# Kernel optimization log

Hardware: AMD Instinct MI355X
Metric: run time of the kernel (lower is better)

## Reference

```python
import jax, jax.numpy as jnp
import numpy as np

N = 50000   # nodes
E = 800000  # random edges (self-loops appended inside reference, as PyG GATConv does)
H = 4       # attention heads
LEAKY_SLOPE = 0.2
BN_EPS = 1e-5


def setup_inputs() -> dict:
    key = jax.random.key(0)
    ks = jax.random.split(key, 24)
    inp = {
        "x": jax.random.normal(ks[0], (N, 128), jnp.float32),
        "edge_index": jax.random.randint(ks[1], (2, E), 0, N, dtype=jnp.int64),
    }
    # layer dims: (in, out_per_head); concat -> out width = H*out
    dims = [(128, 64), (256, 64), (256, 32)]
    i = 2
    for l, (fin, c) in enumerate(dims, start=1):
        sc = 1.0 / np.sqrt(fin)
        inp[f"W{l}"] = jax.random.normal(ks[i], (fin, H * c), jnp.float32) * sc; i += 1
        inp[f"a_src{l}"] = jax.random.normal(ks[i], (H, c), jnp.float32) * 0.1; i += 1
        inp[f"a_dst{l}"] = jax.random.normal(ks[i], (H, c), jnp.float32) * 0.1; i += 1
        inp[f"b{l}"] = jnp.zeros((H * c,), jnp.float32)
    # batch norm params for the two non-final layers (width = 64*4 = 256)
    for l in (1, 2):
        inp[f"gamma{l}"] = jnp.ones((256,), jnp.float32)
        inp[f"beta{l}"] = jnp.zeros((256,), jnp.float32)
    return inp


def _gat_layer(x, src, dst, W, a_src, a_dst, b, heads):
    n = x.shape[0]
    h = (x @ W).reshape(n, heads, -1)                      # [N,H,C]
    al_s = jnp.sum(h * a_src, axis=-1)                     # [N,H]
    al_d = jnp.sum(h * a_dst, axis=-1)                     # [N,H]
    e = jax.nn.leaky_relu(al_s[src] + al_d[dst], LEAKY_SLOPE)  # [Etot,H]
    # numerically-stable edge softmax over incoming edges per destination
    m = jax.ops.segment_max(e, dst, num_segments=n)
    e = jnp.exp(e - m[dst])
    s = jax.ops.segment_sum(e, dst, num_segments=n)
    alpha = e / (s[dst] + 1e-16)                           # [Etot,H]
    msg = alpha[:, :, None] * h[src]                       # [Etot,H,C]
    out = jax.ops.segment_sum(msg, dst, num_segments=n)    # [N,H,C]
    out = out.reshape(n, -1) + b
    return jax.nn.relu(out)  # GAT_NET applies relu after conv


def _batch_norm(x, gamma, beta):
    mean = jnp.mean(x, axis=0)
    var = jnp.var(x, axis=0)  # biased, matches torch BN training normalization
    return (x - mean) * jax.lax.rsqrt(var + BN_EPS) * gamma + beta


def reference(x, edge_index, W1, a_src1, a_dst1, b1, gamma1, beta1,
              W2, a_src2, a_dst2, b2, gamma2, beta2,
              W3, a_src3, a_dst3, b3):
    n = x.shape[0]
    loop = jnp.arange(n, dtype=edge_index.dtype)
    src = jnp.concatenate([edge_index[0], loop])  # add self-loops (PyG default)
    dst = jnp.concatenate([edge_index[1], loop])

    h = _gat_layer(x, src, dst, W1, a_src1, a_dst1, b1, H)
    # outer F.relu is a no-op after GAT_NET's internal relu, kept implicitly
    h = _batch_norm(h, gamma1, beta1)

    h = _gat_layer(h, src, dst, W2, a_src2, a_dst2, b2, H)
    h = _batch_norm(h, gamma2, beta2)

    return _gat_layer(h, src, dst, W3, a_src3, a_dst3, b3, H)
```

## Files before the change

### kernel.cpp

```cpp
#include <hip/hip_runtime.h>
#include <hip/hip_bf16.h>

constexpr int NN   = 50000;
constexpr int EE   = 800000;
constexpr int ETOT = EE + NN;
constexpr int NP   = 50048;
constexpr int NBLK = (NN + 255) / 256;
constexpr float SLOPE  = 0.2f;
constexpr float EPS_BN = 1e-5f;

typedef __attribute__((ext_vector_type(8))) short bf16x8;
typedef __attribute__((ext_vector_type(4))) float f32x4;

__device__ inline float bf2f(unsigned short u) {
    union { unsigned int i; float f; } c; c.i = ((unsigned int)u) << 16; return c.f;
}

__device__ inline void gload16(const __hip_bfloat16* g, __hip_bfloat16* l) {
    __builtin_amdgcn_global_load_lds(
        (const __attribute__((address_space(1))) unsigned int*)g,
        (__attribute__((address_space(3))) unsigned int*)l, 16, 0, 0);
}


__global__ __launch_bounds__(256) void count_kernel(const int* __restrict__ ei,
                                                    int* __restrict__ cnt) {
    int j = blockIdx.x * 256 + threadIdx.x;
    if (j >= ETOT) return;
    int dst = (j < EE) ? ei[EE + j] : (j - EE);
    atomicAdd(&cnt[dst], 1);
}

__global__ __launch_bounds__(256) void scanA_kernel(const int* __restrict__ cnt,
                                                    int* __restrict__ off,
                                                    int* __restrict__ bsum) {
    int b = blockIdx.x, t = threadIdx.x;
    int i = b * 256 + t;
    int v = (i < NN) ? cnt[i] : 0;
    int lane = t & 63, w = t >> 6;
    int x = v;
    #pragma unroll
    for (int o = 1; o < 64; o <<= 1) { int y = __shfl_up(x, o); if (lane >= o) x += y; }
    __shared__ int ws[4];
    if (lane == 63) ws[w] = x;
    __syncthreads();
    int wo = 0;
    for (int k = 0; k < w; ++k) wo += ws[k];
    int incl = x + wo;
    if (i < NN) off[i] = incl - v;
    if (t == 255) bsum[b] = incl;
}

__global__ __launch_bounds__(256) void scanB_kernel(const int* __restrict__ bsum,
                                                    int* __restrict__ bexc,
                                                    int* __restrict__ off) {
    int t = threadIdx.x;
    int v = (t < NBLK) ? bsum[t] : 0;
    int lane = t & 63, w = t >> 6;
    int x = v;
    #pragma unroll
    for (int o = 1; o < 64; o <<= 1) { int y = __shfl_up(x, o); if (lane >= o) x += y; }
    __shared__ int ws[4];
    if (lane == 63) ws[w] = x;
    __syncthreads();
    int wo = 0;
    for (int k = 0; k < w; ++k) wo += ws[k];
    int incl = x + wo;
    if (t < NBLK) bexc[t] = incl - v;
    if (t == 255) off[NN] = incl;
}

__global__ __launch_bounds__(256) void scanC_kernel(const int* __restrict__ bexc,
                                                    int* __restrict__ off,
                                                    int* __restrict__ cur) {
    int i = blockIdx.x * 256 + threadIdx.x;
    if (i >= NN) return;
    int v = off[i] + bexc[blockIdx.x];
    off[i] = v;
    cur[i] = v;
}

__global__ __launch_bounds__(256) void fill_kernel(const int* __restrict__ ei,
                                                   int* __restrict__ cursor,
                                                   int* __restrict__ ssrc) {
    int j = blockIdx.x * 256 + threadIdx.x;
    if (j >= ETOT) return;
    int src, dst;
    if (j < EE) { src = ei[j]; dst = ei[EE + j]; }
    else        { src = dst = j - EE; }
    int pos = atomicAdd(&cursor[dst], 1);
    ssrc[pos] = src;
}

constexpr int XB = (int)(((long)NP * 128 / 8 + 255) / 256);
__global__ __launch_bounds__(256) void castwx_kernel(const float* __restrict__ X,
                                                     const float* __restrict__ W,
                                                     __hip_bfloat16* __restrict__ Xbf,
                                                     __hip_bfloat16* __restrict__ WT) {
    int b = blockIdx.x;
    if (b < XB) {
        long e0 = ((long)b * 256 + threadIdx.x) * 8;
        if (e0 >= (long)NP * 128) return;
        int row = (int)(e0 / 128);
        __hip_bfloat16 o[8];
        if (row < NN) {
            float4 v0 = *reinterpret_cast<const float4*>(X + e0);
            float4 v1 = *reinterpret_cast<const float4*>(X + e0 + 4);
            o[0] = __float2bfloat16(v0.x); o[1] = __float2bfloat16(v0.y);
            o[2] = __float2bfloat16(v0.z); o[3] = __float2bfloat16(v0.w);
            o[4] = __float2bfloat16(v1.x); o[5] = __float2bfloat16(v1.y);
            o[6] = __float2bfloat16(v1.z); o[7] = __float2bfloat16(v1.w);
        } else {
            for (int j = 0; j < 8; ++j) o[j] = __float2bfloat16(0.f);
        }
        *reinterpret_cast<bf16x8*>(Xbf + e0) = *reinterpret_cast<bf16x8*>(o);
    } else {
        int i = (b - XB) * 256 + threadIdx.x;
        int c = i / 128, k = i % 128;
        WT[i] = __float2bfloat16(W[(size_t)k * 256 + c]);
    }
}

template <int WOUT>
__global__ __launch_bounds__(256) void foldw_kernel(const float* __restrict__ W,
                                                    const float* __restrict__ sums,
                                                    const float* __restrict__ gamma,
                                                    const float* __restrict__ beta,
                                                    __hip_bfloat16* __restrict__ WTp,
                                                    float* __restrict__ bb) {
    int c = blockIdx.x, k = threadIdx.x;
    float mean = sums[k] / (float)NN;
    float var  = sums[256 + k] / (float)NN - mean * mean;
    float inv  = rsqrtf(var + EPS_BN);
    float sc   = gamma[k] * inv;
    float sh   = beta[k] - mean * sc;
    float w = W[(size_t)k * WOUT + c];
    WTp[(size_t)c * 256 + k] = __float2bfloat16(sc * w);
    float p = sh * w;
    #pragma unroll
    for (int o = 1; o < 64; o <<= 1) p += __shfl_xor(p, o);
    __shared__ float ps[4];
    if ((k & 63) == 0) ps[k >> 6] = p;
    __syncthreads();
    if (k == 0) bb[c] = ps[0] + ps[1] + ps[2] + ps[3];
}

template <int FIN, int WOUT, bool FOLD>
__global__ __launch_bounds__(256) void mgemm_kernel(const __hip_bfloat16* __restrict__ A,
                                                    const __hip_bfloat16* __restrict__ BT,
                                                    const float* __restrict__ bb,
                                                    const float* __restrict__ a_src,
                                                    const float* __restrict__ a_dst,
                                                    __hip_bfloat16* __restrict__ Hbf,
                                                    float* __restrict__ als,
                                                    float* __restrict__ ald) {
    __shared__ __hip_bfloat16 As[128 * 32];
    __shared__ __hip_bfloat16 Bs[128 * 32];
    int t = threadIdx.x;
    int lane = t & 63, w = t >> 6;
    int row0 = blockIdx.x * 128;
    int col0 = blockIdx.y * 128;
    int wr = w >> 1, wc = w & 1;

    f32x4 acc[4][4];
    #pragma unroll
    for (int m = 0; m < 4; ++m)
        #pragma unroll
        for (int n = 0; n < 4; ++n) acc[m][n] = (f32x4){0.f, 0.f, 0.f, 0.f};

    int srow = w * 32 + (lane >> 2);
    int sbc  = (lane & 3) * 8;
    const __hip_bfloat16* gA0 = A  + (size_t)(row0 + srow)      * FIN + sbc;
    const __hip_bfloat16* gA1 = A  + (size_t)(row0 + srow + 16) * FIN + sbc;
    const __hip_bfloat16* gB0 = BT + (size_t)(col0 + srow)      * FIN + sbc;
    const __hip_bfloat16* gB1 = BT + (size_t)(col0 + srow + 16) * FIN + sbc;
    __hip_bfloat16* lA0 = As + w * 1024;
    __hip_bfloat16* lA1 = As + w * 1024 + 512;
    __hip_bfloat16* lB0 = Bs + w * 1024;
    __hip_bfloat16* lB1 = Bs + w * 1024 + 512;

    int rA = (wr * 64 + (lane & 15)) * 32 + (lane >> 4) * 8;
    int rB = (wc * 64 + (lane & 15)) * 32 + (lane >> 4) * 8;

    for (int k0 = 0; k0 < FIN; k0 += 32) {
        gload16(gA0 + k0, lA0);
        gload16(gA1 + k0, lA1);
        gload16(gB0 + k0, lB0);
        gload16(gB1 + k0, lB1);
        __syncthreads();
        bf16x8 af[4], bfr[4];
        #pragma unroll
        for (int m = 0; m < 4; ++m) af[m]  = *reinterpret_cast<const bf16x8*>(As + rA + m * 16 * 32);
        #pragma unroll
        for (int n = 0; n < 4; ++n) bfr[n] = *reinterpret_cast<const bf16x8*>(Bs + rB + n * 16 * 32);
        #pragma unroll
        for (int m = 0; m < 4; ++m)
            #pragma unroll
            for (int n = 0; n < 4; ++n)
                acc[m][n] = __builtin_amdgcn_mfma_f32_16x16x32_bf16(af[m], bfr[n], acc[m][n], 0, 0, 0);
        __syncthreads();
    }

    int cih = lane & 15;

    if constexpr (FOLD) {
        #pragma unroll
        for (int n = 0; n < 4; ++n) {
            float badd = bb[col0 + wc * 64 + n * 16 + cih];
            #pragma unroll
            for (int m = 0; m < 4; ++m)
                #pragma unroll
                for (int j = 0; j < 4; ++j) acc[m][n][j] += badd;
        }
    }

    float asv[4], adv[4];
    int headw = 0;
    if constexpr (WOUT == 256) {
        headw = (col0 >> 6) + wc;
        #pragma unroll
        for (int n = 0; n < 4; ++n) {
            asv[n] = a_src[headw * 64 + n * 16 + cih];
            adv[n] = a_dst[headw * 64 + n * 16 + cih];
        }
    } else {
        #pragma unroll
        for (int n = 0; n < 4; ++n) {
            int hh = wc * 2 + (n >> 1);
            asv[n] = a_src[hh * 32 + (n & 1) * 16 + cih];
            adv[n] = a_dst[hh * 32 + (n & 1) * 16 + cih];
        }
    }

    #pragma unroll
    for (int m = 0; m < 4; ++m) {
        #pragma unroll
        for (int j = 0; j < 4; ++j) {
            int r = row0 + wr * 64 + m * 16 + (lane >> 4) * 4 + j;
            if constexpr (WOUT == 256) {
                float vs = acc[m][0][j] * asv[0] + acc[m][1][j] * asv[1]
                         + acc[m][2][j] * asv[2] + acc[m][3][j] * asv[3];
                float vd = acc[m][0][j] * adv[0] + acc[m][1][j] * adv[1]
                         + acc[m][2][j] * adv[2] + acc[m][3][j] * adv[3];
                #pragma unroll
                for (int o = 1; o < 16; o <<= 1) {
                    vs += __shfl_xor(vs, o);
                    vd += __shfl_xor(vd, o);
                }
                if (cih == 0) {
                    als[(size_t)r * 4 + headw] = vs;
                    ald[(size_t)r * 4 + headw] = vd;
                }
            } else {
                float vs0 = acc[m][0][j] * asv[0] + acc[m][1][j] * asv[1];
                float vs1 = acc[m][2][j] * asv[2] + acc[m][3][j] * asv[3];
                float vd0 = acc[m][0][j] * adv[0] + acc[m][1][j] * adv[1];
                float vd1 = acc[m][2][j] * adv[2] + acc[m][3][j] * adv[3];
                #pragma unroll
                for (int o = 1; o < 16; o <<= 1) {
                    vs0 += __shfl_xor(vs0, o); vs1 += __shfl_xor(vs1, o);
                    vd0 += __shfl_xor(vd0, o); vd1 += __shfl_xor(vd1, o);
                }
                if (cih == 0) {
                    als[(size_t)r * 4 + wc * 2]     = vs0;
                    als[(size_t)r * 4 + wc * 2 + 1] = vs1;
                    ald[(size_t)r * 4 + wc * 2]     = vd0;
                    ald[(size_t)r * 4 + wc * 2 + 1] = vd1;
                }
            }
        }
    }

    #pragma unroll
    for (int n = 0; n < 4; ++n) {
        int c = col0 + wc * 64 + n * 16 + cih;
        #pragma unroll
        for (int m = 0; m < 4; ++m) {
            int r = row0 + wr * 64 + m * 16 + (lane >> 4) * 4;
            #pragma unroll
            for (int j = 0; j < 4; ++j)
                Hbf[(size_t)(r + j) * WOUT + c] = __float2bfloat16(acc[m][n][j]);
        }
    }
}

__global__ __launch_bounds__(256) void attn256_kernel(const __hip_bfloat16* __restrict__ Hm,
                                                      const int* __restrict__ off,
                                                      const int* __restrict__ ssrc,
                                                      const float* __restrict__ als,
                                                      const float* __restrict__ ald,
                                                      const float* __restrict__ bias,
                                                      __hip_bfloat16* __restrict__ Out) {
    int wid  = threadIdx.x >> 6;
    int lane = threadIdx.x & 63;
    int g    = lane >> 4;
    int q    = lane & 15;
    int d    = blockIdx.x * 16 + wid * 4 + g;
    int hA   = q >> 3;

    int e0 = off[d], e1 = off[d + 1];
    float aldA = ald[(size_t)d * 4 + hA];
    float aldB = ald[(size_t)d * 4 + hA + 2];

    float accA[8], accB[8];
    #pragma unroll
    for (int c = 0; c < 8; ++c) { accA[c] = 0.f; accB[c] = 0.f; }
    float denA = 0.f, denB = 0.f;

    int j = e0;
    for (; j + 3 < e1; j += 4) {
        int s0 = ssrc[j], s1 = ssrc[j + 1], s2 = ssrc[j + 2], s3 = ssrc[j + 3];
        const __hip_bfloat16* r0 = Hm + (size_t)s0 * 256 + q * 8;
        const __hip_bfloat16* r1 = Hm + (size_t)s1 * 256 + q * 8;
        const __hip_bfloat16* r2 = Hm + (size_t)s2 * 256 + q * 8;
        const __hip_bfloat16* r3 = Hm + (size_t)s3 * 256 + q * 8;
        bf16x8 a0 = *reinterpret_cast<const bf16x8*>(r0);
        bf16x8 b0 = *reinterpret_cast<const bf16x8*>(r0 + 128);
        bf16x8 a1 = *reinterpret_cast<const bf16x8*>(r1);
        bf16x8 b1 = *reinterpret_cast<const bf16x8*>(r1 + 128);
        bf16x8 a2 = *reinterpret_cast<const bf16x8*>(r2);
        bf16x8 b2 = *reinterpret_cast<const bf16x8*>(r2 + 128);
        bf16x8 a3 = *reinterpret_cast<const bf16x8*>(r3);
        bf16x8 b3 = *reinterpret_cast<const bf16x8*>(r3 + 128);
        float xA0 = als[(size_t)s0 * 4 + hA] + aldA, xB0 = als[(size_t)s0 * 4 + hA + 2] + aldB;
        float xA1 = als[(size_t)s1 * 4 + hA] + aldA, xB1 = als[(size_t)s1 * 4 + hA + 2] + aldB;
        float xA2 = als[(size_t)s2 * 4 + hA] + aldA, xB2 = als[(size_t)s2 * 4 + hA + 2] + aldB;
        float xA3 = als[(size_t)s3 * 4 + hA] + aldA, xB3 = als[(size_t)s3 * 4 + hA + 2] + aldB;
        xA0 = (xA0 > 0.f) ? xA0 : SLOPE * xA0;  xB0 = (xB0 > 0.f) ? xB0 : SLOPE * xB0;
        xA1 = (xA1 > 0.f) ? xA1 : SLOPE * xA1;  xB1 = (xB1 > 0.f) ? xB1 : SLOPE * xB1;
        xA2 = (xA2 > 0.f) ? xA2 : SLOPE * xA2;  xB2 = (xB2 > 0.f) ? xB2 : SLOPE * xB2;
        xA3 = (xA3 > 0.f) ? xA3 : SLOPE * xA3;  xB3 = (xB3 > 0.f) ? xB3 : SLOPE * xB3;
        float wA0 = __expf(xA0), wB0 = __expf(xB0);
        float wA1 = __expf(xA1), wB1 = __expf(xB1);
        float wA2 = __expf(xA2), wB2 = __expf(xB2);
        float wA3 = __expf(xA3), wB3 = __expf(xB3);
        denA += (wA0 + wA1) + (wA2 + wA3);
        denB += (wB0 + wB1) + (wB2 + wB3);
        #pragma unroll
        for (int c = 0; c < 8; ++c) {
            accA[c] += wA0 * bf2f((unsigned short)a0[c]) + wA1 * bf2f((unsigned short)a1[c])
                     + wA2 * bf2f((unsigned short)a2[c]) + wA3 * bf2f((unsigned short)a3[c]);
            accB[c] += wB0 * bf2f((unsigned short)b0[c]) + wB1 * bf2f((unsigned short)b1[c])
                     + wB2 * bf2f((unsigned short)b2[c]) + wB3 * bf2f((unsigned short)b3[c]);
        }
    }
    for (; j < e1; ++j) {
        int s0 = ssrc[j];
        const __hip_bfloat16* r0 = Hm + (size_t)s0 * 256 + q * 8;
        bf16x8 a0 = *reinterpret_cast<const bf16x8*>(r0);
        bf16x8 b0 = *reinterpret_cast<const bf16x8*>(r0 + 128);
        float xA0 = als[(size_t)s0 * 4 + hA] + aldA, xB0 = als[(size_t)s0 * 4 + hA + 2] + aldB;
        xA0 = (xA0 > 0.f) ? xA0 : SLOPE * xA0;  xB0 = (xB0 > 0.f) ? xB0 : SLOPE * xB0;
        float wA0 = __expf(xA0), wB0 = __expf(xB0);
        denA += wA0; denB += wB0;
        #pragma unroll
        for (int c = 0; c < 8; ++c) {
            accA[c] += wA0 * bf2f((unsigned short)a0[c]);
            accB[c] += wB0 * bf2f((unsigned short)b0[c]);
        }
    }

    float invA = 1.f / (denA + 1e-16f);
    float invB = 1.f / (denB + 1e-16f);

    float4 bA0 = *reinterpret_cast<const float4*>(bias + q * 8);
    float4 bA1 = *reinterpret_cast<const float4*>(bias + q * 8 + 4);
    float4 bB0 = *reinterpret_cast<const float4*>(bias + 128 + q * 8);
    float4 bB1 = *reinterpret_cast<const float4*>(bias + 128 + q * 8 + 4);
    __hip_bfloat16 oA[8], oB[8];
    oA[0] = __float2bfloat16(fmaxf(accA[0] * invA + bA0.x, 0.f));
    oA[1] = __float2bfloat16(fmaxf(accA[1] * invA + bA0.y, 0.f));
    oA[2] = __float2bfloat16(fmaxf(accA[2] * invA + bA0.z, 0.f));
    oA[3] = __float2bfloat16(fmaxf(accA[3] * invA + bA0.w, 0.f));
    oA[4] = __float2bfloat16(fmaxf(accA[4] * invA + bA1.x, 0.f));
    oA[5] = __float2bfloat16(fmaxf(accA[5] * invA + bA1.y, 0.f));
    oA[6] = __float2bfloat16(fmaxf(accA[6] * invA + bA1.z, 0.f));
    oA[7] = __float2bfloat16(fmaxf(accA[7] * invA + bA1.w, 0.f));
    oB[0] = __float2bfloat16(fmaxf(accB[0] * invB + bB0.x, 0.f));
    oB[1] = __float2bfloat16(fmaxf(accB[1] * invB + bB0.y, 0.f));
    oB[2] = __float2bfloat16(fmaxf(accB[2] * invB + bB0.z, 0.f));
    oB[3] = __float2bfloat16(fmaxf(accB[3] * invB + bB0.w, 0.f));
    oB[4] = __float2bfloat16(fmaxf(accB[4] * invB + bB1.x, 0.f));
    oB[5] = __float2bfloat16(fmaxf(accB[5] * invB + bB1.y, 0.f));
    oB[6] = __float2bfloat16(fmaxf(accB[6] * invB + bB1.z, 0.f));
    oB[7] = __float2bfloat16(fmaxf(accB[7] * invB + bB1.w, 0.f));
    __hip_bfloat16* op = Out + (size_t)d * 256 + q * 8;
    *reinterpret_cast<bf16x8*>(op)       = *reinterpret_cast<bf16x8*>(oA);
    *reinterpret_cast<bf16x8*>(op + 128) = *reinterpret_cast<bf16x8*>(oB);
}

__global__ __launch_bounds__(256) void attn128_kernel(const __hip_bfloat16* __restrict__ Hm,
                                                      const int* __restrict__ off,
                                                      const int* __restrict__ ssrc,
                                                      const float* __restrict__ als,
                                                      const float* __restrict__ ald,
                                                      const float* __restrict__ bias,
                                                      float* __restrict__ Out) {
    int wid  = threadIdx.x >> 6;
    int lane = threadIdx.x & 63;
    int g    = lane >> 4;
    int q    = lane & 15;
    int d    = blockIdx.x * 16 + wid * 4 + g;
    int head = q >> 2;

    int e0 = off[d], e1 = off[d + 1];
    float aldh = ald[(size_t)d * 4 + head];

    float acc[8];
    #pragma unroll
    for (int c = 0; c < 8; ++c) acc[c] = 0.f;
    float den = 0.f;

    int j = e0;
    for (; j + 3 < e1; j += 4) {
        int s0 = ssrc[j], s1 = ssrc[j + 1], s2 = ssrc[j + 2], s3 = ssrc[j + 3];
        bf16x8 a0 = *reinterpret_cast<const bf16x8*>(Hm + (size_t)s0 * 128 + q * 8);
        bf16x8 a1 = *reinterpret_cast<const bf16x8*>(Hm + (size_t)s1 * 128 + q * 8);
        bf16x8 a2 = *reinterpret_cast<const bf16x8*>(Hm + (size_t)s2 * 128 + q * 8);
        bf16x8 a3 = *reinterpret_cast<const bf16x8*>(Hm + (size_t)s3 * 128 + q * 8);
        float x0 = als[(size_t)s0 * 4 + head] + aldh;
        float x1 = als[(size_t)s1 * 4 + head] + aldh;
        float x2 = als[(size_t)s2 * 4 + head] + aldh;
        float x3 = als[(size_t)s3 * 4 + head] + aldh;
        x0 = (x0 > 0.f) ? x0 : SLOPE * x0;
        x1 = (x1 > 0.f) ? x1 : SLOPE * x1;
        x2 = (x2 > 0.f) ? x2 : SLOPE * x2;
        x3 = (x3 > 0.f) ? x3 : SLOPE * x3;
        float w0 = __expf(x0), w1 = __expf(x1), w2 = __expf(x2), w3 = __expf(x3);
        den += (w0 + w1) + (w2 + w3);
        #pragma unroll
        for (int c = 0; c < 8; ++c)
            acc[c] += w0 * bf2f((unsigned short)a0[c]) + w1 * bf2f((unsigned short)a1[c])
                    + w2 * bf2f((unsigned short)a2[c]) + w3 * bf2f((unsigned short)a3[c]);
    }
    for (; j < e1; ++j) {
        int s0 = ssrc[j];
        bf16x8 a0 = *reinterpret_cast<const bf16x8*>(Hm + (size_t)s0 * 128 + q * 8);
        float x0 = als[(size_t)s0 * 4 + head] + aldh;
        x0 = (x0 > 0.f) ? x0 : SLOPE * x0;
        float w0 = __expf(x0);
        den += w0;
        #pragma unroll
        for (int c = 0; c < 8; ++c) acc[c] += w0 * bf2f((unsigned short)a0[c]);
    }

    float inv = 1.f / (den + 1e-16f);
    float4 b0 = *reinterpret_cast<const float4*>(bias + q * 8);
    float4 b1 = *reinterpret_cast<const float4*>(bias + q * 8 + 4);
    float* op = Out + (size_t)d * 128 + q * 8;
    *reinterpret_cast<float4*>(op) = make_float4(
        fmaxf(acc[0] * inv + b0.x, 0.f), fmaxf(acc[1] * inv + b0.y, 0.f),
        fmaxf(acc[2] * inv + b0.z, 0.f), fmaxf(acc[3] * inv + b0.w, 0.f));
    *reinterpret_cast<float4*>(op + 4) = make_float4(
        fmaxf(acc[4] * inv + b1.x, 0.f), fmaxf(acc[5] * inv + b1.y, 0.f),
        fmaxf(acc[6] * inv + b1.z, 0.f), fmaxf(acc[7] * inv + b1.w, 0.f));
}

__global__ __launch_bounds__(256) void bnstats_kernel(const __hip_bfloat16* __restrict__ X,
                                                      float* __restrict__ sums) {
    int c  = threadIdx.x;
    int r0 = blockIdx.x * 200;
    float s = 0.f, q = 0.f;
    for (int r = r0; r < r0 + 200; ++r) {
        float v = bf2f(*(const unsigned short*)(X + (size_t)r * 256 + c));
        s += v; q += v * v;
    }
    atomicAdd(&sums[c], s);
    atomicAdd(&sums[256 + c], q);
}


extern "C" void kernel_launch(void* const* d_in, const int* in_sizes, int n_in,
                              void* d_out, int out_size, void* d_ws, size_t ws_size,
                              hipStream_t stream) {
    const float* x      = (const float*)d_in[0];
    const int*   ei     = (const int*)d_in[1];
    const float* W1     = (const float*)d_in[2];
    const float* a_s1   = (const float*)d_in[3];
    const float* a_d1   = (const float*)d_in[4];
    const float* b1     = (const float*)d_in[5];
    const float* W2     = (const float*)d_in[6];
    const float* a_s2   = (const float*)d_in[7];
    const float* a_d2   = (const float*)d_in[8];
    const float* b2     = (const float*)d_in[9];
    const float* W3     = (const float*)d_in[10];
    const float* a_s3   = (const float*)d_in[11];
    const float* a_d3   = (const float*)d_in[12];
    const float* b3     = (const float*)d_in[13];
    const float* gamma1 = (const float*)d_in[14];
    const float* beta1  = (const float*)d_in[15];
    const float* gamma2 = (const float*)d_in[16];
    const float* beta2  = (const float*)d_in[17];

    char* ws = (char*)d_ws;
    size_t o = 0;
    auto alloc = [&](size_t bytes) -> void* {
        void* p = ws + o;
        o = (o + bytes + 255) & ~size_t(255);
        return p;
    };
    __hip_bfloat16*  Abf  = (__hip_bfloat16*)alloc((size_t)NP * 256 * 2);
    __hip_bfloat16*  Hbf  = (__hip_bfloat16*)alloc((size_t)NP * 256 * 2);
    __hip_bfloat16*  Xbf  = (__hip_bfloat16*)alloc((size_t)NP * 128 * 2);
    __hip_bfloat16*  WT1  = (__hip_bfloat16*)alloc((size_t)256 * 128 * 2);
    __hip_bfloat16*  WT2  = (__hip_bfloat16*)alloc((size_t)256 * 256 * 2);
    __hip_bfloat16*  WT3  = (__hip_bfloat16*)alloc((size_t)128 * 256 * 2);
    float* bb2   = (float*)alloc(256 * 4);
    float* bb3   = (float*)alloc(128 * 4);
    float* als   = (float*)alloc((size_t)NP * 4 * 4);
    float* ald   = (float*)alloc((size_t)NP * 4 * 4);
    float* sums  = (float*)alloc(512 * 4);
    int*   off   = (int*)alloc((size_t)(NN + 1) * 4);
    int*   cur   = (int*)alloc((size_t)NN * 4);
    int*   cnt   = (int*)alloc((size_t)NN * 4);
    int*   bsum  = (int*)alloc((size_t)NBLK * 4);
    int*   bexc  = (int*)alloc((size_t)NBLK * 4);
    int*   ssrc  = (int*)alloc((size_t)ETOT * 4);
    (void)ws_size; (void)in_sizes; (void)n_in; (void)out_size;

    const int EB = (ETOT + 255) / 256;

    hipMemsetAsync(cnt, 0, (size_t)NN * 4, stream);
    count_kernel<<<EB, 256, 0, stream>>>(ei, cnt);
    scanA_kernel<<<NBLK, 256, 0, stream>>>(cnt, off, bsum);
    scanB_kernel<<<1, 256, 0, stream>>>(bsum, bexc, off);
    scanC_kernel<<<NBLK, 256, 0, stream>>>(bexc, off, cur);
    fill_kernel<<<EB, 256, 0, stream>>>(ei, cur, ssrc);

    castwx_kernel<<<XB + 128, 256, 0, stream>>>(x, W1, Xbf, WT1);
    mgemm_kernel<128, 256, false><<<dim3(NP / 128, 2), 256, 0, stream>>>(
        Xbf, WT1, nullptr, a_s1, a_d1, Hbf, als, ald);
    attn256_kernel<<<NN / 16, 256, 0, stream>>>(Hbf, off, ssrc, als, ald, b1, Abf);

    hipMemsetAsync(sums, 0, 512 * 4, stream);
    bnstats_kernel<<<250, 256, 0, stream>>>(Abf, sums);
    foldw_kernel<256><<<256, 256, 0, stream>>>(W2, sums, gamma1, beta1, WT2, bb2);

    mgemm_kernel<256, 256, true><<<dim3(NP / 128, 2), 256, 0, stream>>>(
        Abf, WT2, bb2, a_s2, a_d2, Hbf, als, ald);
    attn256_kernel<<<NN / 16, 256, 0, stream>>>(Hbf, off, ssrc, als, ald, b2, Abf);

    hipMemsetAsync(sums, 0, 512 * 4, stream);
    bnstats_kernel<<<250, 256, 0, stream>>>(Abf, sums);
    foldw_kernel<128><<<128, 256, 0, stream>>>(W3, sums, gamma2, beta2, WT3, bb3);

    mgemm_kernel<256, 128, true><<<dim3(NP / 128, 1), 256, 0, stream>>>(
        Abf, WT3, bb3, a_s3, a_d3, Hbf, als, ald);
    attn128_kernel<<<NN / 16, 256, 0, stream>>>(Hbf, off, ssrc, als, ald, b3, (float*)d_out);
}
```

Measured before the change: 382.1 us.

## Store GEMM output in column panels and split attention aggregation by panel

The GEMM epilogue now writes H into 8 column panels (32 or 16 bf16 wide), each stored contiguously across nodes. The attention kernels get a 2D grid where blockIdx.x selects the panel. Within a wave, the edges of one destination are spread across lanes and combined with a shuffle reduction. The intent is that each panel (about 3.2 MB) fits in cache, so the random source-row gathers hit L2/MALL instead of DRAM, and that lanes parallelise over edges instead of looping serially. In exchange, the per-edge index and attention-logit loads and exp computations are repeated for every panel, and the reductions add shuffle overhead.

After: 696.6 us. 1.82x slower.

```diff
diff --git a/kernel.cpp b/kernel.cpp
--- a/kernel.cpp
+++ b/kernel.cpp
@@ -151,9 +151,10 @@
                                                     const float* __restrict__ bb,
                                                     const float* __restrict__ a_src,
                                                     const float* __restrict__ a_dst,
-                                                    __hip_bfloat16* __restrict__ Hbf,
+                                                    __hip_bfloat16* __restrict__ Hpan,
                                                     float* __restrict__ als,
                                                     float* __restrict__ ald) {
+    constexpr int PW = (WOUT == 256) ? 32 : 16;
     __shared__ __hip_bfloat16 As[128 * 32];
     __shared__ __hip_bfloat16 Bs[128 * 32];
     int t = threadIdx.x;
@@ -274,186 +275,141 @@
     #pragma unroll
     for (int n = 0; n < 4; ++n) {
         int c = col0 + wc * 64 + n * 16 + cih;
+        int p = c / PW;
+        int cw = c % PW;
         #pragma unroll
         for (int m = 0; m < 4; ++m) {
             int r = row0 + wr * 64 + m * 16 + (lane >> 4) * 4;
             #pragma unroll
             for (int j = 0; j < 4; ++j)
-                Hbf[(size_t)(r + j) * WOUT + c] = __float2bfloat16(acc[m][n][j]);
-        }
-    }
-}
-
-__global__ __launch_bounds__(256) void attn256_kernel(const __hip_bfloat16* __restrict__ Hm,
-                                                      const int* __restrict__ off,
-                                                      const int* __restrict__ ssrc,
-                                                      const float* __restrict__ als,
-                                                      const float* __restrict__ ald,
-                                                      const float* __restrict__ bias,
-                                                      __hip_bfloat16* __restrict__ Out) {
-    int wid  = threadIdx.x >> 6;
+                Hpan[(size_t)p * NP * PW + (size_t)(r + j) * PW + cw] =
+                    __float2bfloat16(acc[m][n][j]);
+        }
+    }
+}
+
+__global__ __launch_bounds__(256) void attn256s_kernel(const __hip_bfloat16* __restrict__ Hpan,
+                                                       const int* __restrict__ off,
+                                                       const int* __restrict__ ssrc,
+                                                       const float* __restrict__ als,
+                                                       const float* __restrict__ ald,
+                                                       const float* __restrict__ bias,
+                                                       __hip_bfloat16* __restrict__ Out) {
+    int s    = blockIdx.x;
+    int wv   = threadIdx.x >> 6;
     int lane = threadIdx.x & 63;
-    int g    = lane >> 4;
-    int q    = lane & 15;
-    int d    = blockIdx.x * 16 + wid * 4 + g;
-    int hA   = q >> 3;
-
-    int e0 = off[d], e1 = off[d + 1];
-    float aldA = ald[(size_t)d * 4 + hA];
-    float aldB = ald[(size_t)d * 4 + hA + 2];
-
-    float accA[8], accB[8];
-    #pragma unroll
-    for (int c = 0; c < 8; ++c) { accA[c] = 0.f; accB[c] = 0.f; }
-    float denA = 0.f, denB = 0.f;
-
-    int j = e0;
-    for (; j + 3 < e1; j += 4) {
-        int s0 = ssrc[j], s1 = ssrc[j + 1], s2 = ssrc[j + 2], s3 = ssrc[j + 3];
-        const __hip_bfloat16* r0 = Hm + (size_t)s0 * 256 + q * 8;
-        const __hip_bfloat16* r1 = Hm + (size_t)s1 * 256 + q * 8;
-        const __hip_bfloat16* r2 = Hm + (size_t)s2 * 256 + q * 8;
-        const __hip_bfloat16* r3 = Hm + (size_t)s3 * 256 + q * 8;
-        bf16x8 a0 = *reinterpret_cast<const bf16x8*>(r0);
-        bf16x8 b0 = *reinterpret_cast<const bf16x8*>(r0 + 128);
-        bf16x8 a1 = *reinterpret_cast<const bf16x8*>(r1);
-        bf16x8 b1 = *reinterpret_cast<const bf16x8*>(r1 + 128);
-        bf16x8 a2 = *reinterpret_cast<const bf16x8*>(r2);
-        bf16x8 b2 = *reinterpret_cast<const bf16x8*>(r2 + 128);
-        bf16x8 a3 = *reinterpret_cast<const bf16x8*>(r3);
-        bf16x8 b3 = *reinterpret_cast<const bf16x8*>(r3 + 128);
-        float xA0 = als[(size_t)s0 * 4 + hA] + aldA, xB0 = als[(size_t)s0 * 4 + hA + 2] + aldB;
-        float xA1 = als[(size_t)s1 * 4 + hA] + aldA, xB1 = als[(size_t)s1 * 4 + hA + 2] + aldB;
-        float xA2 = als[(size_t)s2 * 4 + hA] + aldA, xB2 = als[(size_t)s2 * 4 + hA + 2] + aldB;
-        float xA3 = als[(size_t)s3 * 4 + hA] + aldA, xB3 = als[(size_t)s3 * 4 + hA + 2] + aldB;
-        xA0 = (xA0 > 0.f) ? xA0 : SLOPE * xA0;  xB0 = (xB0 > 0.f) ? xB0 : SLOPE * xB0;
-        xA1 = (xA1 > 0.f) ? xA1 : SLOPE * xA1;  xB1 = (xB1 > 0.f) ? xB1 : SLOPE * xB1;
-        xA2 = (xA2 > 0.f) ? xA2 : SLOPE * xA2;  xB2 = (xB2 > 0.f) ? xB2 : SLOPE * xB2;
-        xA3 = (xA3 > 0.f) ? xA3 : SLOPE * xA3;  xB3 = (xB3 > 0.f) ? xB3 : SLOPE * xB3;
-        float wA0 = __expf(xA0), wB0 = __expf(xB0);
-        float wA1 = __expf(xA1), wB1 = __expf(xB1);
-        float wA2 = __expf(xA2), wB2 = __expf(xB2);
-        float wA3 = __expf(xA3), wB3 = __expf(xB3);
-        denA += (wA0 + wA1) + (wA2 + wA3);
-        denB += (wB0 + wB1) + (wB2 + wB3);
-        #pragma unroll
-        for (int c = 0; c < 8; ++c) {
-            accA[c] += wA0 * bf2f((unsigned short)a0[c]) + wA1 * bf2f((unsigned short)a1[c])
-                     + wA2 * bf2f((unsigned short)a2[c]) + wA3 * bf2f((unsigned short)a3[c]);
-            accB[c] += wB0 * bf2f((unsigned short)b0[c]) + wB1 * bf2f((unsigned short)b1[c])
-                     + wB2 * bf2f((unsigned short)b2[c]) + wB3 * bf2f((unsigned short)b3[c]);
-        }
-    }
-    for (; j < e1; ++j) {
-        int s0 = ssrc[j];
-        const __hip_bfloat16* r0 = Hm + (size_t)s0 * 256 + q * 8;
-        bf16x8 a0 = *reinterpret_cast<const bf16x8*>(r0);
-        bf16x8 b0 = *reinterpret_cast<const bf16x8*>(r0 + 128);
-        float xA0 = als[(size_t)s0 * 4 + hA] + aldA, xB0 = als[(size_t)s0 * 4 + hA + 2] + aldB;
-        xA0 = (xA0 > 0.f) ? xA0 : SLOPE * xA0;  xB0 = (xB0 > 0.f) ? xB0 : SLOPE * xB0;
-        float wA0 = __expf(xA0), wB0 = __expf(xB0);
-        denA += wA0; denB += wB0;
-        #pragma unroll
-        for (int c = 0; c < 8; ++c) {
-            accA[c] += wA0 * bf2f((unsigned short)a0[c]);
-            accB[c] += wB0 * bf2f((unsigned short)b0[c]);
-        }
-    }
-
-    float invA = 1.f / (denA + 1e-16f);
-    float invB = 1.f / (denB + 1e-16f);
-
-    float4 bA0 = *reinterpret_cast<const float4*>(bias + q * 8);
-    float4 bA1 = *reinterpret_cast<const float4*>(bias + q * 8 + 4);
-    float4 bB0 = *reinterpret_cast<const float4*>(bias + 128 + q * 8);
-    float4 bB1 = *reinterpret_cast<const float4*>(bias + 128 + q * 8 + 4);
-    __hip_bfloat16 oA[8], oB[8];
-    oA[0] = __float2bfloat16(fmaxf(accA[0] * invA + bA0.x, 0.f));
-    oA[1] = __float2bfloat16(fmaxf(accA[1] * invA + bA0.y, 0.f));
-    oA[2] = __float2bfloat16(fmaxf(accA[2] * invA + bA0.z, 0.f));
-    oA[3] = __float2bfloat16(fmaxf(accA[3] * invA + bA0.w, 0.f));
-    oA[4] = __float2bfloat16(fmaxf(accA[4] * invA + bA1.x, 0.f));
-    oA[5] = __float2bfloat16(fmaxf(accA[5] * invA + bA1.y, 0.f));
-    oA[6] = __float2bfloat16(fmaxf(accA[6] * invA + bA1.z, 0.f));
-    oA[7] = __float2bfloat16(fmaxf(accA[7] * invA + bA1.w, 0.f));
-    oB[0] = __float2bfloat16(fmaxf(accB[0] * invB + bB0.x, 0.f));
-    oB[1] = __float2bfloat16(fmaxf(accB[1] * invB + bB0.y, 0.f));
-    oB[2] = __float2bfloat16(fmaxf(accB[2] * invB + bB0.z, 0.f));
-    oB[3] = __float2bfloat16(fmaxf(accB[3] * invB + bB0.w, 0.f));
-    oB[4] = __float2bfloat16(fmaxf(accB[4] * invB + bB1.x, 0.f));
-    oB[5] = __float2bfloat16(fmaxf(accB[5] * invB + bB1.y, 0.f));
-    oB[6] = __float2bfloat16(fmaxf(accB[6] * invB + bB1.z, 0.f));
-    oB[7] = __float2bfloat16(fmaxf(accB[7] * invB + bB1.w, 0.f));
-    __hip_bfloat16* op = Out + (size_t)d * 256 + q * 8;
-    *reinterpret_cast<bf16x8*>(op)       = *reinterpret_cast<bf16x8*>(oA);
-    *reinterpret_cast<bf16x8*>(op + 128) = *reinterpret_cast<bf16x8*>(oB);
-}
-
-__global__ __launch_bounds__(256) void attn128_kernel(const __hip_bfloat16* __restrict__ Hm,
-                                                      const int* __restrict__ off,
-                                                      const int* __restrict__ ssrc,
-                                                      const float* __restrict__ als,
-                                                      const float* __restrict__ ald,
-                                                      const float* __restrict__ bias,
-                                                      float* __restrict__ Out) {
-    int wid  = threadIdx.x >> 6;
+    int cl   = lane >> 2;
+    int sub  = lane & 3;
+    int head = s >> 1;
+    const __hip_bfloat16* Hp = Hpan + (size_t)s * NP * 32;
+
+    float4 bia0 = *reinterpret_cast<const float4*>(bias + s * 32 + sub * 8);
+    float4 bia1 = *reinterpret_cast<const float4*>(bias + s * 32 + sub * 8 + 4);
+
+    #pragma unroll
+    for (int k = 0; k < 4; ++k) {
+        int d = blockIdx.y * 16 + wv * 4 + k;
+        int e0 = off[d], e1 = off[d + 1];
+        float aldh = ald[(size_t)d * 4 + head];
+
+        float acc[8];
+        #pragma unroll
+        for (int c = 0; c < 8; ++c) acc[c] = 0.f;
+        float den = 0.f;
+
+        for (int j = e0 + cl; j < e1; j += 16) {
+            int src = ssrc[j];
+            float x = als[(size_t)src * 4 + head] + aldh;
+            x = (x > 0.f) ? x : SLOPE * x;
+            float wgt = __expf(x);
+            den += wgt;
+            bf16x8 v = *reinterpret_cast<const bf16x8*>(Hp + (size_t)src * 32 + sub * 8);
+            #pragma unroll
+            for (int c = 0; c < 8; ++c) acc[c] += wgt * bf2f((unsigned short)v[c]);
+        }
+
+        #pragma unroll
+        for (int o = 4; o < 64; o <<= 1) {
+            #pragma unroll
+            for (int c = 0; c < 8; ++c) acc[c] += __shfl_xor(acc[c], o);
+            den += __shfl_xor(den, o);
+        }
+        float inv = 1.f / (den + 1e-16f);
+
+        if (cl == 0) {
+            __hip_bfloat16 ob[8];
+            ob[0] = __float2bfloat16(fmaxf(acc[0] * inv + bia0.x, 0.f));
+            ob[1] = __float2bfloat16(fmaxf(acc[1] * inv + bia0.y, 0.f));
+            ob[2] = __float2bfloat16(fmaxf(acc[2] * inv + bia0.z, 0.f));
+            ob[3] = __float2bfloat16(fmaxf(acc[3] * inv + bia0.w, 0.f));
+            ob[4] = __float2bfloat16(fmaxf(acc[4] * inv + bia1.x, 0.f));
+            ob[5] = __float2bfloat16(fmaxf(acc[5] * inv + bia1.y, 0.f));
+            ob[6] = __float2bfloat16(fmaxf(acc[6] * inv + bia1.z, 0.f));
+            ob[7] = __float2bfloat16(fmaxf(acc[7] * inv + bia1.w, 0.f));
+            *reinterpret_cast<bf16x8*>(Out + (size_t)d * 256 + s * 32 + sub * 8) =
+                *reinterpret_cast<bf16x8*>(ob);
+        }
+    }
+}
+
+__global__ __launch_bounds__(256) void attn128s_kernel(const __hip_bfloat16* __restrict__ Hpan,
+                                                       const int* __restrict__ off,
+                                                       const int* __restrict__ ssrc,
+                                                       const float* __restrict__ als,
+                                                       const float* __restrict__ ald,
+                                                       const float* __restrict__ bias,
+                                                       float* __restrict__ Out) {
+    int s    = blockIdx.x;
+    int wv   = threadIdx.x >> 6;
     int lane = threadIdx.x & 63;
-    int g    = lane >> 4;
-    int q    = lane & 15;
-    int d    = blockIdx.x * 16 + wid * 4 + g;
-    int head = q >> 2;
-
-    int e0 = off[d], e1 = off[d + 1];
-    float aldh = ald[(size_t)d * 4 + head];
-
-    float acc[8];
-    #pragma unroll
-    for (int c = 0; c < 8; ++c) acc[c] = 0.f;
-    float den = 0.f;
-
-    int j = e0;
-    for (; j + 3 < e1; j += 4) {
-        int s0 = ssrc[j], s1 = ssrc[j + 1], s2 = ssrc[j + 2], s3 = ssrc[j + 3];
-        bf16x8 a0 = *reinterpret_cast<const bf16x8*>(Hm + (size_t)s0 * 128 + q * 8);
-        bf16x8 a1 = *reinterpret_cast<const bf16x8*>(Hm + (size_t)s1 * 128 + q * 8);
-        bf16x8 a2 = *reinterpret_cast<const bf16x8*>(Hm + (size_t)s2 * 128 + q * 8);
-        bf16x8 a3 = *reinterpret_cast<const bf16x8*>(Hm + (size_t)s3 * 128 + q * 8);
-        float x0 = als[(size_t)s0 * 4 + head] + aldh;
-        float x1 = als[(size_t)s1 * 4 + head] + aldh;
-        float x2 = als[(size_t)s2 * 4 + head] + aldh;
-        float x3 = als[(size_t)s3 * 4 + head] + aldh;
-        x0 = (x0 > 0.f) ? x0 : SLOPE * x0;
-        x1 = (x1 > 0.f) ? x1 : SLOPE * x1;
-        x2 = (x2 > 0.f) ? x2 : SLOPE * x2;
-        x3 = (x3 > 0.f) ? x3 : SLOPE * x3;
-        float w0 = __expf(x0), w1 = __expf(x1), w2 = __expf(x2), w3 = __expf(x3);
-        den += (w0 + w1) + (w2 + w3);
-        #pragma unroll
-        for (int c = 0; c < 8; ++c)
-            acc[c] += w0 * bf2f((unsigned short)a0[c]) + w1 * bf2f((unsigned short)a1[c])
-                    + w2 * bf2f((unsigned short)a2[c]) + w3 * bf2f((unsigned short)a3[c]);
-    }
-    for (; j < e1; ++j) {
-        int s0 = ssrc[j];
-        bf16x8 a0 = *reinterpret_cast<const bf16x8*>(Hm + (size_t)s0 * 128 + q * 8);
-        float x0 = als[(size_t)s0 * 4 + head] + aldh;
-        x0 = (x0 > 0.f) ? x0 : SLOPE * x0;
-        float w0 = __expf(x0);
-        den += w0;
-        #pragma unroll
-        for (int c = 0; c < 8; ++c) acc[c] += w0 * bf2f((unsigned short)a0[c]);
-    }
-
-    float inv = 1.f / (den + 1e-16f);
-    float4 b0 = *reinterpret_cast<const float4*>(bias + q * 8);
-    float4 b1 = *reinterpret_cast<const float4*>(bias + q * 8 + 4);
-    float* op = Out + (size_t)d * 128 + q * 8;
-    *reinterpret_cast<float4*>(op) = make_float4(
-        fmaxf(acc[0] * inv + b0.x, 0.f), fmaxf(acc[1] * inv + b0.y, 0.f),
-        fmaxf(acc[2] * inv + b0.z, 0.f), fmaxf(acc[3] * inv + b0.w, 0.f));
-    *reinterpret_cast<float4*>(op + 4) = make_float4(
-        fmaxf(acc[4] * inv + b1.x, 0.f), fmaxf(acc[5] * inv + b1.y, 0.f),
-        fmaxf(acc[6] * inv + b1.z, 0.f), fmaxf(acc[7] * inv + b1.w, 0.f));
+    int cl   = lane >> 1;
+    int sub  = lane & 1;
+    int head = s >> 1;
+    const __hip_bfloat16* Hp = Hpan + (size_t)s * NP * 16;
+
+    float4 bia0 = *reinterpret_cast<const float4*>(bias + s * 16 + sub * 8);
+    float4 bia1 = *reinterpret_cast<const float4*>(bias + s * 16 + sub * 8 + 4);
+
+    #pragma unroll
+    for (int k = 0; k < 4; ++k) {
+        int d = blockIdx.y * 16 + wv * 4 + k;
+        int e0 = off[d], e1 = off[d + 1];
+        float aldh = ald[(size_t)d * 4 + head];
+
+        float acc[8];
+        #pragma unroll
+        for (int c = 0; c < 8; ++c) acc[c] = 0.f;
+        float den = 0.f;
+
+        for (int j = e0 + cl; j < e1; j += 32) {
+            int src = ssrc[j];
+            float x = als[(size_t)src * 4 + head] + aldh;
+            x = (x > 0.f) ? x : SLOPE * x;
+            float wgt = __expf(x);
+            den += wgt;
+            bf16x8 v = *reinterpret_cast<const bf16x8*>(Hp + (size_t)src * 16 + sub * 8);
+            #pragma unroll
+            for (int c = 0; c < 8; ++c) acc[c] += wgt * bf2f((unsigned short)v[c]);
+        }
+
+        #pragma unroll
+        for (int o = 2; o < 64; o <<= 1) {
+            #pragma unroll
+            for (int c = 0; c < 8; ++c) acc[c] += __shfl_xor(acc[c], o);
+            den += __shfl_xor(den, o);
+        }
+        float inv = 1.f / (den + 1e-16f);
+
+        if (cl == 0) {
+            float* op = Out + (size_t)d * 128 + s * 16 + sub * 8;
+            *reinterpret_cast<float4*>(op) = make_float4(
+                fmaxf(acc[0] * inv + bia0.x, 0.f), fmaxf(acc[1] * inv + bia0.y, 0.f),
+                fmaxf(acc[2] * inv + bia0.z, 0.f), fmaxf(acc[3] * inv + bia0.w, 0.f));
+            *reinterpret_cast<float4*>(op + 4) = make_float4(
+                fmaxf(acc[4] * inv + bia1.x, 0.f), fmaxf(acc[5] * inv + bia1.y, 0.f),
+                fmaxf(acc[6] * inv + bia1.z, 0.f), fmaxf(acc[7] * inv + bia1.w, 0.f));
+        }
+    }
 }
 
 __global__ __launch_bounds__(256) void bnstats_kernel(const __hip_bfloat16* __restrict__ X,
@@ -530,7 +486,7 @@
     castwx_kernel<<<XB + 128, 256, 0, stream>>>(x, W1, Xbf, WT1);
     mgemm_kernel<128, 256, false><<<dim3(NP / 128, 2), 256, 0, stream>>>(
         Xbf, WT1, nullptr, a_s1, a_d1, Hbf, als, ald);
-    attn256_kernel<<<NN / 16, 256, 0, stream>>>(Hbf, off, ssrc, als, ald, b1, Abf);
+    attn256s_kernel<<<dim3(8, NN / 16), 256, 0, stream>>>(Hbf, off, ssrc, als, ald, b1, Abf);
 
     hipMemsetAsync(sums, 0, 512 * 4, stream);
     bnstats_kernel<<<250, 256, 0, stream>>>(Abf, sums);
@@ -538,7 +494,7 @@
 
     mgemm_kernel<256, 256, true><<<dim3(NP / 128, 2), 256, 0, stream>>>(
         Abf, WT2, bb2, a_s2, a_d2, Hbf, als, ald);
-    attn256_kernel<<<NN / 16, 256, 0, stream>>>(Hbf, off, ssrc, als, ald, b2, Abf);
+    attn256s_kernel<<<dim3(8, NN / 16), 256, 0, stream>>>(Hbf, off, ssrc, als, ald, b2, Abf);
 
     hipMemsetAsync(sums, 0, 512 * 4, stream);
     bnstats_kernel<<<250, 256, 0, stream>>>(Abf, sums);
@@ -546,5 +502,5 @@
 
     mgemm_kernel<256, 128, true><<<dim3(NP / 128, 1), 256, 0, stream>>>(
         Abf, WT3, bb3, a_s3, a_d3, Hbf, als, ald);
-    attn128_kernel<<<NN / 16, 256, 0, stream>>>(Hbf, off, ssrc, als, ald, b3, (float*)d_out);
-}
+    attn128s_kernel<<<dim3(8, NN / 16), 256, 0, stream>>>(Hbf, off, ssrc, als, ald, b3, (float*)d_out);
+}
```
